# Performance work log

Hardware: AMD Instinct MI355X
Metric: run time of the kernel (lower is better)

## Reference

```python
import jax, jax.numpy as jnp
import numpy as np

N, D = 4096, 32


def setup_inputs() -> dict:
    key = jax.random.key(0)
    k1, _ = jax.random.split(key)
    particles = jax.random.normal(k1, (N, D), dtype=jnp.float32)
    length_scale = jnp.ones((1,), dtype=jnp.float32)
    return {"particles": particles, "length_scale": length_scale}


def reference(particles, length_scale):
    # SVGDModel.calculate_gradient with an RBF kernel and standard-Gaussian density.
    num_particles = particles.shape[0]
    ls2 = length_scale[0] ** 2

    # pairwise differences: diff[i, j] = x_i - x_j  -> [N, N, D]
    diff = particles[:, None, :] - particles[None, :, :]
    sq_dists = jnp.sum(diff * diff, axis=-1)               # [N, N]

    # gram_matrix = k(x_i, x_j) = exp(-||x_i - x_j||^2 / (2 l^2))
    gram_matrix = jnp.exp(-sq_dists / (2.0 * ls2))          # [N, N]

    # density.score for standard Gaussian: grad log p(x) = -x
    score_matrix = -particles                               # [N, D]

    # kernel_gradient[i, j] = grad_{x_i} k(x_i, x_j) = -(x_i - x_j)/l^2 * k
    kernel_gradient = -(diff / ls2) * gram_matrix[..., None]  # [N, N, D]

    kernel_score_term = jnp.einsum('ij,jk->ik', gram_matrix, score_matrix)  # [N, D]
    kernel_gradient_term = jnp.sum(kernel_gradient, axis=0)                 # [N, D]

    phi = (kernel_score_term + kernel_gradient_term) / num_particles
    return phi
```

## Files before the change

kernel.cpp:

```cpp
#include <hip/hip_runtime.h>

#define NPART 4096
#define DIM 32
#define LOG2E 1.44269504088896340736f

typedef _Float16 f16x8 __attribute__((ext_vector_type(8)));
typedef _Float16 f16x4 __attribute__((ext_vector_type(4)));
typedef float f32x4 __attribute__((ext_vector_type(4)));

__global__ __launch_bounds__(256) void svgd_prep_kernel(
    const float* __restrict__ X, const float* __restrict__ ls,
    float* __restrict__ m2, _Float16* __restrict__ XhP,
    _Float16* __restrict__ XlP, _Float16* __restrict__ XT,
    float* __restrict__ out) {
  const int row = blockIdx.x * 256 + threadIdx.x;

  {
    float4 z = make_float4(0.f, 0.f, 0.f, 0.f);
    float4* o4 = reinterpret_cast<float4*>(out);
#pragma unroll
    for (int q = 0; q < 8; ++q) o4[(size_t)q * 4096 + row] = z;
  }

  float v[DIM];
  const float4* xr = reinterpret_cast<const float4*>(X + (size_t)row * DIM);
#pragma unroll
  for (int q = 0; q < 8; ++q) {
    float4 a = xr[q];
    v[4 * q + 0] = a.x; v[4 * q + 1] = a.y; v[4 * q + 2] = a.z; v[4 * q + 3] = a.w;
  }
  float n = 0.f;
#pragma unroll
  for (int d = 0; d < DIM; ++d) n = fmaf(v[d], v[d], n);
  const float lsv = ls[0];
  const float inv = 1.f / (lsv * lsv);
  m2[row] = n * (0.5f * inv) * LOG2E;

  _Float16 h[DIM], l[DIM];
#pragma unroll
  for (int d = 0; d < DIM; ++d) {
    h[d] = (_Float16)v[d];
    l[d] = (_Float16)(v[d] - (float)h[d]);
  }
#pragma unroll
  for (int g = 0; g < 4; ++g) {
    f16x8 ph, pl;
#pragma unroll
    for (int e = 0; e < 8; ++e) {
      int d = (e < 4) ? (4 * g + e) : (16 + 4 * g + (e - 4));
      ph[e] = h[d];
      pl[e] = l[d];
    }
    *reinterpret_cast<f16x8*>(XhP + (size_t)row * DIM + g * 8) = ph;
    *reinterpret_cast<f16x8*>(XlP + (size_t)row * DIM + g * 8) = pl;
  }
#pragma unroll
  for (int d = 0; d < DIM; ++d) XT[(size_t)d * NPART + row] = h[d];
}

__global__ __launch_bounds__(256, 4) void svgd_fused_kernel(
    const float* __restrict__ X, const _Float16* __restrict__ XhP,
    const _Float16* __restrict__ XlP, const _Float16* __restrict__ XT,
    const float* __restrict__ ls, const float* __restrict__ m2,
    float* __restrict__ out) {
  __shared__ float sT[4][32][32];
  __shared__ float sS[4][32];

  const int tid = threadIdx.x;
  const int lane = tid & 63;
  const int g = lane >> 4;
  const int li = lane & 15;
  const int wave = tid >> 6;
  const int i0 = blockIdx.x * 32;
  const int jbase = blockIdx.y * 512 + wave * 128;

  const float lsv = ls[0];
  const float si2 = LOG2E / (lsv * lsv);

  f16x8 bh0, bl0, bh1, bl1;
  float mi0, mi1;
  {
    const int r0 = i0 + li, r1 = i0 + 16 + li;
    bh0 = *reinterpret_cast<const f16x8*>(XhP + (size_t)r0 * DIM + g * 8);
    bl0 = *reinterpret_cast<const f16x8*>(XlP + (size_t)r0 * DIM + g * 8);
    bh1 = *reinterpret_cast<const f16x8*>(XhP + (size_t)r1 * DIM + g * 8);
    bl1 = *reinterpret_cast<const f16x8*>(XlP + (size_t)r1 * DIM + g * 8);
    mi0 = m2[r0];
    mi1 = m2[r1];
  }

  f32x4 c2a0 = {0.f, 0.f, 0.f, 0.f}, c2b0 = {0.f, 0.f, 0.f, 0.f};
  f32x4 c2a1 = {0.f, 0.f, 0.f, 0.f}, c2b1 = {0.f, 0.f, 0.f, 0.f};
  float Sp0 = 0.f, Sp1 = 0.f;

  f16x8 Ah0, Al0, Ah1, Al1;
  f16x4 Ba0, Bb0, Ba1, Bb1;
  float4 Mj0, Mj1;

  auto LOADJ = [&](int j0, f16x8& Ah, f16x8& Al, f16x4& Ba, f16x4& Bb,
                   float4& Mj) {
    Ah = *reinterpret_cast<const f16x8*>(XhP + (size_t)(j0 + li) * DIM + g * 8);
    Al = *reinterpret_cast<const f16x8*>(XlP + (size_t)(j0 + li) * DIM + g * 8);
    Ba = *reinterpret_cast<const f16x4*>(XT + (size_t)li * NPART + j0 + 4 * g);
    Bb = *reinterpret_cast<const f16x4*>(XT + (size_t)(16 + li) * NPART + j0 + 4 * g);
    Mj = *reinterpret_cast<const float4*>(m2 + j0 + 4 * g);
  };

  auto COMP = [&](const f16x8& Ah, const f16x8& Al, const f16x4& Ba,
                  const f16x4& Bb, const float4& Mj) {
    f32x4 c10 = {0.f, 0.f, 0.f, 0.f}, c11 = {0.f, 0.f, 0.f, 0.f};
    c10 = __builtin_amdgcn_mfma_f32_16x16x32_f16(Ah, bh0, c10, 0, 0, 0);
    c11 = __builtin_amdgcn_mfma_f32_16x16x32_f16(Ah, bh1, c11, 0, 0, 0);
    c10 = __builtin_amdgcn_mfma_f32_16x16x32_f16(Al, bh0, c10, 0, 0, 0);
    c11 = __builtin_amdgcn_mfma_f32_16x16x32_f16(Al, bh1, c11, 0, 0, 0);
    c10 = __builtin_amdgcn_mfma_f32_16x16x32_f16(Ah, bl0, c10, 0, 0, 0);
    c11 = __builtin_amdgcn_mfma_f32_16x16x32_f16(Ah, bl1, c11, 0, 0, 0);
    const float mj[4] = {Mj.x, Mj.y, Mj.z, Mj.w};
    f16x4 a20, a21;
#pragma unroll
    for (int r = 0; r < 4; ++r) {
      float k0 = exp2f(fmaf(c10[r], si2, -(mi0 + mj[r])));
      float k1 = exp2f(fmaf(c11[r], si2, -(mi1 + mj[r])));
      Sp0 += k0;
      Sp1 += k1;
      a20[r] = (_Float16)k0;
      a21[r] = (_Float16)k1;
    }
    c2a0 = __builtin_amdgcn_mfma_f32_16x16x16f16(a20, Ba, c2a0, 0, 0, 0);
    c2b0 = __builtin_amdgcn_mfma_f32_16x16x16f16(a20, Bb, c2b0, 0, 0, 0);
    c2a1 = __builtin_amdgcn_mfma_f32_16x16x16f16(a21, Ba, c2a1, 0, 0, 0);
    c2b1 = __builtin_amdgcn_mfma_f32_16x16x16f16(a21, Bb, c2b1, 0, 0, 0);
  };

  LOADJ(jbase, Ah0, Al0, Ba0, Bb0, Mj0);
#pragma unroll
  for (int itr = 0; itr < 8; itr += 2) {
    LOADJ(jbase + (itr + 1) * 16, Ah1, Al1, Ba1, Bb1, Mj1);
    COMP(Ah0, Al0, Ba0, Bb0, Mj0);
    const int jn2 = jbase + ((itr + 2 < 8) ? (itr + 2) * 16 : 0);
    LOADJ(jn2, Ah0, Al0, Ba0, Bb0, Mj0);
    COMP(Ah1, Al1, Ba1, Bb1, Mj1);
  }

#pragma unroll
  for (int r = 0; r < 4; ++r) {
    sT[wave][4 * g + r][li] = c2a0[r];
    sT[wave][4 * g + r][16 + li] = c2b0[r];
    sT[wave][16 + 4 * g + r][li] = c2a1[r];
    sT[wave][16 + 4 * g + r][16 + li] = c2b1[r];
  }
  {
    float s0 = Sp0, s1 = Sp1;
    s0 += __shfl_xor(s0, 16, 64);
    s0 += __shfl_xor(s0, 32, 64);
    s1 += __shfl_xor(s1, 16, 64);
    s1 += __shfl_xor(s1, 32, 64);
    if (g == 0) {
      sS[wave][li] = s0;
      sS[wave][16 + li] = s1;
    }
  }
  __syncthreads();

  const float inv = si2 * (1.f / LOG2E);
  const float c1f = inv * (1.f / NPART);
  const float c2f = (1.f + inv) * (1.f / NPART);
#pragma unroll
  for (int q = 0; q < 4; ++q) {
    const int v = q * 256 + tid;
    const int row = v >> 5, d = v & 31;
    const float T = sT[0][row][d] + sT[1][row][d] + sT[2][row][d] + sT[3][row][d];
    const float S = sS[0][row] + sS[1][row] + sS[2][row] + sS[3][row];
    const size_t idx = (size_t)(i0 + row) * DIM + d;
    unsafeAtomicAdd(&out[idx], c1f * S * X[idx] - c2f * T);
  }
}

#define TJ 64
__global__ __launch_bounds__(256) void svgd_direct_kernel(const float* __restrict__ X,
                                                          const float* __restrict__ ls,
                                                          float* __restrict__ out) {
  __shared__ float4 sX[TJ * 8];
  const int tid = threadIdx.x;
  const int row = blockIdx.x * 256 + tid;
  const float lsv = ls[0];
  const float ls2 = lsv * lsv;
  const float inv2 = 0.5f / ls2;
  float4 xi[8];
  const float4* xr = reinterpret_cast<const float4*>(X + (size_t)row * DIM);
#pragma unroll
  for (int q = 0; q < 8; ++q) xi[q] = xr[q];
  float4 acc[8];
#pragma unroll
  for (int q = 0; q < 8; ++q) acc[q] = make_float4(0.f, 0.f, 0.f, 0.f);
  float S = 0.f;
  for (int jb = 0; jb < NPART; jb += TJ) {
    __syncthreads();
    const float4* src = reinterpret_cast<const float4*>(X + (size_t)jb * DIM);
    for (int t = tid; t < TJ * 8; t += 256) sX[t] = src[t];
    __syncthreads();
    for (int t = 0; t < TJ; ++t) {
      const float4* xj = &sX[t * 8];
      float4 v[8];
      float d0 = 0.f, d1 = 0.f, d2 = 0.f, d3 = 0.f;
#pragma unroll
      for (int q = 0; q < 8; ++q) {
        v[q] = xj[q];
        float ax = xi[q].x - v[q].x; d0 = fmaf(ax, ax, d0);
        float ay = xi[q].y - v[q].y; d1 = fmaf(ay, ay, d1);
        float az = xi[q].z - v[q].z; d2 = fmaf(az, az, d2);
        float aw = xi[q].w - v[q].w; d3 = fmaf(aw, aw, d3);
      }
      float k = __expf(-((d0 + d1) + (d2 + d3)) * inv2);
      S += k;
#pragma unroll
      for (int q = 0; q < 8; ++q) {
        acc[q].x = fmaf(k, v[q].x, acc[q].x);
        acc[q].y = fmaf(k, v[q].y, acc[q].y);
        acc[q].z = fmaf(k, v[q].z, acc[q].z);
        acc[q].w = fmaf(k, v[q].w, acc[q].w);
      }
    }
  }
  const float inv = 1.f / ls2;
  const float c1 = inv * S;
  const float c2 = 1.f + inv;
  float4* o = reinterpret_cast<float4*>(out + (size_t)row * DIM);
#pragma unroll
  for (int q = 0; q < 8; ++q) {
    float4 r;
    r.x = (c1 * xi[q].x - c2 * acc[q].x) * (1.f / NPART);
    r.y = (c1 * xi[q].y - c2 * acc[q].y) * (1.f / NPART);
    r.z = (c1 * xi[q].z - c2 * acc[q].z) * (1.f / NPART);
    r.w = (c1 * xi[q].w - c2 * acc[q].w) * (1.f / NPART);
    o[q] = r;
  }
}

extern "C" void kernel_launch(void* const* d_in, const int* in_sizes, int n_in,
                              void* d_out, int out_size, void* d_ws, size_t ws_size,
                              hipStream_t stream) {
  const float* X = (const float*)d_in[0];
  const float* ls = (const float*)d_in[1];
  float* out = (float*)d_out;
  float* ws = (float*)d_ws;

  const size_t fixed = 4096 + 3 * 65536;
  if (4 * fixed > ws_size) {
    svgd_direct_kernel<<<NPART / 256, 256, 0, stream>>>(X, ls, out);
    return;
  }

  float* m2 = ws;
  _Float16* XhP = reinterpret_cast<_Float16*>(ws + 4096);
  _Float16* XlP = XhP + NPART * DIM;
  _Float16* XT = XlP + NPART * DIM;

  svgd_prep_kernel<<<NPART / 256, 256, 0, stream>>>(X, ls, m2, XhP, XlP, XT, out);
  dim3 grid(NPART / 32, 8);
  svgd_fused_kernel<<<grid, 256, 0, stream>>>(X, XhP, XlP, XT, ls, m2, out);
}
```

Before: 27.29 us.

## Fuse prep into main kernel, converting j-tiles to f16 hi/lo in shared memory

Replaces the separate prep kernel with a single-pass kernel. Each block loads its j-tile of fp32 particles, computes the norms and the f16 hi/lo splits plus the transposed copy, and stages them in LDS before doing the MFMA work. The output is zeroed with hipMemsetAsync instead of by the prep kernel. This removes a kernel launch and the workspace round trip, but every block now redoes the conversion work for its j-tile (8x redundancy across blockIdx.x) and adds extra syncthreads per stage.

```diff
diff --git a/kernel.cpp b/kernel.cpp
--- a/kernel.cpp
+++ b/kernel.cpp
@@ -7,6 +7,167 @@
 typedef _Float16 f16x8 __attribute__((ext_vector_type(8)));
 typedef _Float16 f16x4 __attribute__((ext_vector_type(4)));
 typedef float f32x4 __attribute__((ext_vector_type(4)));
+
+__global__ __launch_bounds__(256, 4) void svgd_onepass_kernel(
+    const float* __restrict__ X, const float* __restrict__ ls,
+    float* __restrict__ out) {
+  __shared__ __align__(16) unsigned char smem[26624];
+  _Float16* sHi = (_Float16*)smem;
+  _Float16* sLo = (_Float16*)(smem + 8192);
+  _Float16* sXT = (_Float16*)(smem + 16384);
+  float* sM2 = (float*)(smem + 25088);
+  float* sS = (float*)(smem + 26112);
+  float* sT = (float*)smem;
+
+  const int tid = threadIdx.x;
+  const int lane = tid & 63;
+  const int g = lane >> 4;
+  const int li = lane & 15;
+  const int wave = tid >> 6;
+  const int i0 = blockIdx.x * 32;
+  const int jb0 = blockIdx.y * 512;
+
+  const float lsv = ls[0];
+  const float inv = 1.f / (lsv * lsv);
+  const float si2 = LOG2E * inv;
+  const float hm = 0.5f * si2;
+
+  const float4* X4 = (const float4*)X;
+
+  f16x8 bh0, bl0, bh1, bl1;
+  float mi0, mi1;
+  {
+    const int r0 = i0 + li, r1 = i0 + 16 + li;
+    float4 a0 = X4[(size_t)r0 * 8 + g], b0 = X4[(size_t)r0 * 8 + 4 + g];
+    float4 a1 = X4[(size_t)r1 * 8 + g], b1 = X4[(size_t)r1 * 8 + 4 + g];
+    float t0[8] = {a0.x, a0.y, a0.z, a0.w, b0.x, b0.y, b0.z, b0.w};
+    float t1[8] = {a1.x, a1.y, a1.z, a1.w, b1.x, b1.y, b1.z, b1.w};
+    float n0 = 0.f, n1 = 0.f;
+#pragma unroll
+    for (int e = 0; e < 8; ++e) {
+      n0 = fmaf(t0[e], t0[e], n0);
+      n1 = fmaf(t1[e], t1[e], n1);
+      _Float16 h0 = (_Float16)t0[e];
+      _Float16 h1 = (_Float16)t1[e];
+      bh0[e] = h0; bl0[e] = (_Float16)(t0[e] - (float)h0);
+      bh1[e] = h1; bl1[e] = (_Float16)(t1[e] - (float)h1);
+    }
+    n0 += __shfl_xor(n0, 16, 64);
+    n0 += __shfl_xor(n0, 32, 64);
+    n1 += __shfl_xor(n1, 16, 64);
+    n1 += __shfl_xor(n1, 32, 64);
+    mi0 = n0 * hm;
+    mi1 = n1 * hm;
+  }
+
+  f32x4 c2a0 = {0.f, 0.f, 0.f, 0.f}, c2b0 = {0.f, 0.f, 0.f, 0.f};
+  f32x4 c2a1 = {0.f, 0.f, 0.f, 0.f}, c2b1 = {0.f, 0.f, 0.f, 0.f};
+  float Sp0 = 0.f, Sp1 = 0.f;
+
+#pragma unroll
+  for (int s = 0; s < 4; ++s) {
+    __syncthreads();
+    {
+      const int r = tid >> 1, sub = tid & 1;
+      const int row = jb0 + s * 128 + r;
+      const float4* src = X4 + (size_t)row * 8 + sub * 4;
+      float4 va = src[0], vb = src[1], vc = src[2], vd = src[3];
+      float tv[16] = {va.x, va.y, va.z, va.w, vb.x, vb.y, vb.z, vb.w,
+                      vc.x, vc.y, vc.z, vc.w, vd.x, vd.y, vd.z, vd.w};
+      _Float16 h[16], l[16];
+      float nrm = 0.f;
+#pragma unroll
+      for (int e = 0; e < 16; ++e) {
+        nrm = fmaf(tv[e], tv[e], nrm);
+        _Float16 hh = (_Float16)tv[e];
+        h[e] = hh;
+        l[e] = (_Float16)(tv[e] - (float)hh);
+      }
+      sM2[sub * 128 + r] = nrm * hm;
+#pragma unroll
+      for (int gq = 0; gq < 4; ++gq) {
+        f16x4 ph, pl;
+#pragma unroll
+        for (int e = 0; e < 4; ++e) { ph[e] = h[4 * gq + e]; pl[e] = l[4 * gq + e]; }
+        *(f16x4*)(sHi + r * 32 + gq * 8 + sub * 4) = ph;
+        *(f16x4*)(sLo + r * 32 + gq * 8 + sub * 4) = pl;
+      }
+#pragma unroll
+      for (int e = 0; e < 16; ++e) sXT[(16 * sub + e) * 136 + r] = h[e];
+    }
+    __syncthreads();
+
+#pragma unroll
+    for (int it = 0; it < 2; ++it) {
+      const int jloc = wave * 32 + it * 16;
+      f16x8 Ah = *(const f16x8*)(sHi + (jloc + li) * 32 + g * 8);
+      f16x8 Al = *(const f16x8*)(sLo + (jloc + li) * 32 + g * 8);
+      f16x4 Ba = *(const f16x4*)(sXT + li * 136 + jloc + 4 * g);
+      f16x4 Bb = *(const f16x4*)(sXT + (16 + li) * 136 + jloc + 4 * g);
+      f32x4 Mja = *(const f32x4*)(sM2 + jloc + 4 * g);
+      f32x4 Mjb = *(const f32x4*)(sM2 + 128 + jloc + 4 * g);
+
+      f32x4 c10 = {0.f, 0.f, 0.f, 0.f}, c11 = {0.f, 0.f, 0.f, 0.f};
+      c10 = __builtin_amdgcn_mfma_f32_16x16x32_f16(Ah, bh0, c10, 0, 0, 0);
+      c11 = __builtin_amdgcn_mfma_f32_16x16x32_f16(Ah, bh1, c11, 0, 0, 0);
+      c10 = __builtin_amdgcn_mfma_f32_16x16x32_f16(Al, bh0, c10, 0, 0, 0);
+      c11 = __builtin_amdgcn_mfma_f32_16x16x32_f16(Al, bh1, c11, 0, 0, 0);
+      c10 = __builtin_amdgcn_mfma_f32_16x16x32_f16(Ah, bl0, c10, 0, 0, 0);
+      c11 = __builtin_amdgcn_mfma_f32_16x16x32_f16(Ah, bl1, c11, 0, 0, 0);
+      f16x4 a20, a21;
+#pragma unroll
+      for (int r = 0; r < 4; ++r) {
+        const float mj = Mja[r] + Mjb[r];
+        float k0 = exp2f(fmaf(c10[r], si2, -(mi0 + mj)));
+        float k1 = exp2f(fmaf(c11[r], si2, -(mi1 + mj)));
+        Sp0 += k0;
+        Sp1 += k1;
+        a20[r] = (_Float16)k0;
+        a21[r] = (_Float16)k1;
+      }
+      c2a0 = __builtin_amdgcn_mfma_f32_16x16x16f16(a20, Ba, c2a0, 0, 0, 0);
+      c2b0 = __builtin_amdgcn_mfma_f32_16x16x16f16(a20, Bb, c2b0, 0, 0, 0);
+      c2a1 = __builtin_amdgcn_mfma_f32_16x16x16f16(a21, Ba, c2a1, 0, 0, 0);
+      c2b1 = __builtin_amdgcn_mfma_f32_16x16x16f16(a21, Bb, c2b1, 0, 0, 0);
+    }
+  }
+
+  __syncthreads();
+
+#pragma unroll
+  for (int r = 0; r < 4; ++r) {
+    sT[(wave * 32 + 4 * g + r) * 32 + li] = c2a0[r];
+    sT[(wave * 32 + 4 * g + r) * 32 + 16 + li] = c2b0[r];
+    sT[(wave * 32 + 16 + 4 * g + r) * 32 + li] = c2a1[r];
+    sT[(wave * 32 + 16 + 4 * g + r) * 32 + 16 + li] = c2b1[r];
+  }
+  {
+    float s0 = Sp0, s1 = Sp1;
+    s0 += __shfl_xor(s0, 16, 64);
+    s0 += __shfl_xor(s0, 32, 64);
+    s1 += __shfl_xor(s1, 16, 64);
+    s1 += __shfl_xor(s1, 32, 64);
+    if (g == 0) {
+      sS[wave * 32 + li] = s0;
+      sS[wave * 32 + 16 + li] = s1;
+    }
+  }
+  __syncthreads();
+
+  const float c1f = inv * (1.f / NPART);
+  const float c2f = (1.f + inv) * (1.f / NPART);
+#pragma unroll
+  for (int q = 0; q < 4; ++q) {
+    const int v = q * 256 + tid;
+    const int row = v >> 5, d = v & 31;
+    const float T = sT[(0 * 32 + row) * 32 + d] + sT[(1 * 32 + row) * 32 + d] +
+                    sT[(2 * 32 + row) * 32 + d] + sT[(3 * 32 + row) * 32 + d];
+    const float S = sS[0 * 32 + row] + sS[1 * 32 + row] + sS[2 * 32 + row] +
+                    sS[3 * 32 + row];
+    const size_t idx = (size_t)(i0 + row) * DIM + d;
+    unsafeAtomicAdd(&out[idx], c1f * S * X[idx] - c2f * T);
+  }
+}
 
 __global__ __launch_bounds__(256) void svgd_prep_kernel(
     const float* __restrict__ X, const float* __restrict__ ls,
@@ -14,14 +175,12 @@
     _Float16* __restrict__ XlP, _Float16* __restrict__ XT,
     float* __restrict__ out) {
   const int row = blockIdx.x * 256 + threadIdx.x;
-
   {
     float4 z = make_float4(0.f, 0.f, 0.f, 0.f);
     float4* o4 = reinterpret_cast<float4*>(out);
 #pragma unroll
     for (int q = 0; q < 8; ++q) o4[(size_t)q * 4096 + row] = z;
   }
-
   float v[DIM];
   const float4* xr = reinterpret_cast<const float4*>(X + (size_t)row * DIM);
 #pragma unroll
@@ -35,7 +194,6 @@
   const float lsv = ls[0];
   const float inv = 1.f / (lsv * lsv);
   m2[row] = n * (0.5f * inv) * LOG2E;
-
   _Float16 h[DIM], l[DIM];
 #pragma unroll
   for (int d = 0; d < DIM; ++d) {
@@ -65,7 +223,6 @@
     float* __restrict__ out) {
   __shared__ float sT[4][32][32];
   __shared__ float sS[4][32];
-
   const int tid = threadIdx.x;
   const int lane = tid & 63;
   const int g = lane >> 4;
@@ -73,10 +230,8 @@
   const int wave = tid >> 6;
   const int i0 = blockIdx.x * 32;
   const int jbase = blockIdx.y * 512 + wave * 128;
-
   const float lsv = ls[0];
   const float si2 = LOG2E / (lsv * lsv);
-
   f16x8 bh0, bl0, bh1, bl1;
   float mi0, mi1;
   {
@@ -88,15 +243,12 @@
     mi0 = m2[r0];
     mi1 = m2[r1];
   }
-
   f32x4 c2a0 = {0.f, 0.f, 0.f, 0.f}, c2b0 = {0.f, 0.f, 0.f, 0.f};
   f32x4 c2a1 = {0.f, 0.f, 0.f, 0.f}, c2b1 = {0.f, 0.f, 0.f, 0.f};
   float Sp0 = 0.f, Sp1 = 0.f;
-
   f16x8 Ah0, Al0, Ah1, Al1;
   f16x4 Ba0, Bb0, Ba1, Bb1;
   float4 Mj0, Mj1;
-
   auto LOADJ = [&](int j0, f16x8& Ah, f16x8& Al, f16x4& Ba, f16x4& Bb,
                    float4& Mj) {
     Ah = *reinterpret_cast<const f16x8*>(XhP + (size_t)(j0 + li) * DIM + g * 8);
@@ -105,7 +257,6 @@
     Bb = *reinterpret_cast<const f16x4*>(XT + (size_t)(16 + li) * NPART + j0 + 4 * g);
     Mj = *reinterpret_cast<const float4*>(m2 + j0 + 4 * g);
   };
-
   auto COMP = [&](const f16x8& Ah, const f16x8& Al, const f16x4& Ba,
                   const f16x4& Bb, const float4& Mj) {
     f32x4 c10 = {0.f, 0.f, 0.f, 0.f}, c11 = {0.f, 0.f, 0.f, 0.f};
@@ -131,7 +282,6 @@
     c2a1 = __builtin_amdgcn_mfma_f32_16x16x16f16(a21, Ba, c2a1, 0, 0, 0);
     c2b1 = __builtin_amdgcn_mfma_f32_16x16x16f16(a21, Bb, c2b1, 0, 0, 0);
   };
-
   LOADJ(jbase, Ah0, Al0, Ba0, Bb0, Mj0);
 #pragma unroll
   for (int itr = 0; itr < 8; itr += 2) {
@@ -141,7 +291,6 @@
     LOADJ(jn2, Ah0, Al0, Ba0, Bb0, Mj0);
     COMP(Ah1, Al1, Ba1, Bb1, Mj1);
   }
-
 #pragma unroll
   for (int r = 0; r < 4; ++r) {
     sT[wave][4 * g + r][li] = c2a0[r];
@@ -161,7 +310,6 @@
     }
   }
   __syncthreads();
-
   const float inv = si2 * (1.f / LOG2E);
   const float c1f = inv * (1.f / NPART);
   const float c2f = (1.f + inv) * (1.f / NPART);
@@ -245,18 +393,25 @@
   float* out = (float*)d_out;
   float* ws = (float*)d_ws;
 
+  hipError_t e =
+      hipMemsetAsync(d_out, 0, (size_t)out_size * sizeof(float), stream);
+  if (e == hipSuccess) {
+    dim3 grid(NPART / 32, 8);
+    svgd_onepass_kernel<<<grid, 256, 0, stream>>>(X, ls, out);
+    return;
+  }
+
   const size_t fixed = 4096 + 3 * 65536;
   if (4 * fixed > ws_size) {
     svgd_direct_kernel<<<NPART / 256, 256, 0, stream>>>(X, ls, out);
     return;
   }
-
   float* m2 = ws;
   _Float16* XhP = reinterpret_cast<_Float16*>(ws + 4096);
   _Float16* XlP = XhP + NPART * DIM;
   _Float16* XT = XlP + NPART * DIM;
-
-  svgd_prep_kernel<<<NPART / 256, 256, 0, stream>>>(X, ls, m2, XhP, XlP, XT, out);
+  svgd_prep_kernel<<<NPART / 256, 256, 0, stream>>>(X, ls, m2, XhP, XlP, XT,
+                                                    out);
   dim3 grid(NPART / 32, 8);
   svgd_fused_kernel<<<grid, 256, 0, stream>>>(X, XhP, XlP, XT, ls, m2, out);
 }
```

Measured after the change: 26.63 us. 2.4% less time.

## Fuse fp16 split preprocessing into main kernel via shared-memory staging

Applied to the files above, without the earlier changes.

Drops the separate prep kernel and its workspace buffers. The main kernel now loads raw fp32 particles itself, splits each into hi/lo fp16 parts, computes squared norms, and stages j-tiles plus a transposed copy in shared memory. Output zeroing moves to a memset. The grid is also replicated REP=4 times along y with a 1/REP scale, so every j-block is computed four times and atomically added four times. That buys more blocks at the cost of redundant compute and atomics.

```diff
diff --git a/kernel.cpp b/kernel.cpp
--- a/kernel.cpp
+++ b/kernel.cpp
@@ -8,63 +8,17 @@
 typedef _Float16 f16x4 __attribute__((ext_vector_type(4)));
 typedef float f32x4 __attribute__((ext_vector_type(4)));
 
-__global__ __launch_bounds__(256) void svgd_prep_kernel(
+#define REP 4
+__global__ __launch_bounds__(256, 4) void svgd_onepass_kernel(
     const float* __restrict__ X, const float* __restrict__ ls,
-    float* __restrict__ m2, _Float16* __restrict__ XhP,
-    _Float16* __restrict__ XlP, _Float16* __restrict__ XT,
     float* __restrict__ out) {
-  const int row = blockIdx.x * 256 + threadIdx.x;
-
-  {
-    float4 z = make_float4(0.f, 0.f, 0.f, 0.f);
-    float4* o4 = reinterpret_cast<float4*>(out);
-#pragma unroll
-    for (int q = 0; q < 8; ++q) o4[(size_t)q * 4096 + row] = z;
-  }
-
-  float v[DIM];
-  const float4* xr = reinterpret_cast<const float4*>(X + (size_t)row * DIM);
-#pragma unroll
-  for (int q = 0; q < 8; ++q) {
-    float4 a = xr[q];
-    v[4 * q + 0] = a.x; v[4 * q + 1] = a.y; v[4 * q + 2] = a.z; v[4 * q + 3] = a.w;
-  }
-  float n = 0.f;
-#pragma unroll
-  for (int d = 0; d < DIM; ++d) n = fmaf(v[d], v[d], n);
-  const float lsv = ls[0];
-  const float inv = 1.f / (lsv * lsv);
-  m2[row] = n * (0.5f * inv) * LOG2E;
-
-  _Float16 h[DIM], l[DIM];
-#pragma unroll
-  for (int d = 0; d < DIM; ++d) {
-    h[d] = (_Float16)v[d];
-    l[d] = (_Float16)(v[d] - (float)h[d]);
-  }
-#pragma unroll
-  for (int g = 0; g < 4; ++g) {
-    f16x8 ph, pl;
-#pragma unroll
-    for (int e = 0; e < 8; ++e) {
-      int d = (e < 4) ? (4 * g + e) : (16 + 4 * g + (e - 4));
-      ph[e] = h[d];
-      pl[e] = l[d];
-    }
-    *reinterpret_cast<f16x8*>(XhP + (size_t)row * DIM + g * 8) = ph;
-    *reinterpret_cast<f16x8*>(XlP + (size_t)row * DIM + g * 8) = pl;
-  }
-#pragma unroll
-  for (int d = 0; d < DIM; ++d) XT[(size_t)d * NPART + row] = h[d];
-}
-
-__global__ __launch_bounds__(256, 4) void svgd_fused_kernel(
-    const float* __restrict__ X, const _Float16* __restrict__ XhP,
-    const _Float16* __restrict__ XlP, const _Float16* __restrict__ XT,
-    const float* __restrict__ ls, const float* __restrict__ m2,
-    float* __restrict__ out) {
-  __shared__ float sT[4][32][32];
-  __shared__ float sS[4][32];
+  __shared__ __align__(16) unsigned char smem[26624];
+  _Float16* sHi = (_Float16*)smem;
+  _Float16* sLo = (_Float16*)(smem + 8192);
+  _Float16* sXT = (_Float16*)(smem + 16384);
+  float* sM2 = (float*)(smem + 25088);
+  float* sS = (float*)(smem + 26112);
+  float* sT = (float*)smem;
 
   const int tid = threadIdx.x;
   const int lane = tid & 63;
@@ -72,82 +26,121 @@
   const int li = lane & 15;
   const int wave = tid >> 6;
   const int i0 = blockIdx.x * 32;
-  const int jbase = blockIdx.y * 512 + wave * 128;
+  const int jb0 = (blockIdx.y & 7) * 512;
 
   const float lsv = ls[0];
-  const float si2 = LOG2E / (lsv * lsv);
+  const float inv = 1.f / (lsv * lsv);
+  const float si2 = LOG2E * inv;
+  const float hm = 0.5f * si2;
+
+  const float4* X4 = (const float4*)X;
 
   f16x8 bh0, bl0, bh1, bl1;
   float mi0, mi1;
   {
     const int r0 = i0 + li, r1 = i0 + 16 + li;
-    bh0 = *reinterpret_cast<const f16x8*>(XhP + (size_t)r0 * DIM + g * 8);
-    bl0 = *reinterpret_cast<const f16x8*>(XlP + (size_t)r0 * DIM + g * 8);
-    bh1 = *reinterpret_cast<const f16x8*>(XhP + (size_t)r1 * DIM + g * 8);
-    bl1 = *reinterpret_cast<const f16x8*>(XlP + (size_t)r1 * DIM + g * 8);
-    mi0 = m2[r0];
-    mi1 = m2[r1];
+    float4 a0 = X4[(size_t)r0 * 8 + g], b0 = X4[(size_t)r0 * 8 + 4 + g];
+    float4 a1 = X4[(size_t)r1 * 8 + g], b1 = X4[(size_t)r1 * 8 + 4 + g];
+    float t0[8] = {a0.x, a0.y, a0.z, a0.w, b0.x, b0.y, b0.z, b0.w};
+    float t1[8] = {a1.x, a1.y, a1.z, a1.w, b1.x, b1.y, b1.z, b1.w};
+    float n0 = 0.f, n1 = 0.f;
+#pragma unroll
+    for (int e = 0; e < 8; ++e) {
+      n0 = fmaf(t0[e], t0[e], n0);
+      n1 = fmaf(t1[e], t1[e], n1);
+      _Float16 h0 = (_Float16)t0[e];
+      _Float16 h1 = (_Float16)t1[e];
+      bh0[e] = h0; bl0[e] = (_Float16)(t0[e] - (float)h0);
+      bh1[e] = h1; bl1[e] = (_Float16)(t1[e] - (float)h1);
+    }
+    n0 += __shfl_xor(n0, 16, 64);
+    n0 += __shfl_xor(n0, 32, 64);
+    n1 += __shfl_xor(n1, 16, 64);
+    n1 += __shfl_xor(n1, 32, 64);
+    mi0 = n0 * hm;
+    mi1 = n1 * hm;
   }
 
   f32x4 c2a0 = {0.f, 0.f, 0.f, 0.f}, c2b0 = {0.f, 0.f, 0.f, 0.f};
   f32x4 c2a1 = {0.f, 0.f, 0.f, 0.f}, c2b1 = {0.f, 0.f, 0.f, 0.f};
   float Sp0 = 0.f, Sp1 = 0.f;
 
-  f16x8 Ah0, Al0, Ah1, Al1;
-  f16x4 Ba0, Bb0, Ba1, Bb1;
-  float4 Mj0, Mj1;
-
-  auto LOADJ = [&](int j0, f16x8& Ah, f16x8& Al, f16x4& Ba, f16x4& Bb,
-                   float4& Mj) {
-    Ah = *reinterpret_cast<const f16x8*>(XhP + (size_t)(j0 + li) * DIM + g * 8);
-    Al = *reinterpret_cast<const f16x8*>(XlP + (size_t)(j0 + li) * DIM + g * 8);
-    Ba = *reinterpret_cast<const f16x4*>(XT + (size_t)li * NPART + j0 + 4 * g);
-    Bb = *reinterpret_cast<const f16x4*>(XT + (size_t)(16 + li) * NPART + j0 + 4 * g);
-    Mj = *reinterpret_cast<const float4*>(m2 + j0 + 4 * g);
-  };
-
-  auto COMP = [&](const f16x8& Ah, const f16x8& Al, const f16x4& Ba,
-                  const f16x4& Bb, const float4& Mj) {
-    f32x4 c10 = {0.f, 0.f, 0.f, 0.f}, c11 = {0.f, 0.f, 0.f, 0.f};
-    c10 = __builtin_amdgcn_mfma_f32_16x16x32_f16(Ah, bh0, c10, 0, 0, 0);
-    c11 = __builtin_amdgcn_mfma_f32_16x16x32_f16(Ah, bh1, c11, 0, 0, 0);
-    c10 = __builtin_amdgcn_mfma_f32_16x16x32_f16(Al, bh0, c10, 0, 0, 0);
-    c11 = __builtin_amdgcn_mfma_f32_16x16x32_f16(Al, bh1, c11, 0, 0, 0);
-    c10 = __builtin_amdgcn_mfma_f32_16x16x32_f16(Ah, bl0, c10, 0, 0, 0);
-    c11 = __builtin_amdgcn_mfma_f32_16x16x32_f16(Ah, bl1, c11, 0, 0, 0);
-    const float mj[4] = {Mj.x, Mj.y, Mj.z, Mj.w};
-    f16x4 a20, a21;
-#pragma unroll
-    for (int r = 0; r < 4; ++r) {
-      float k0 = exp2f(fmaf(c10[r], si2, -(mi0 + mj[r])));
-      float k1 = exp2f(fmaf(c11[r], si2, -(mi1 + mj[r])));
-      Sp0 += k0;
-      Sp1 += k1;
-      a20[r] = (_Float16)k0;
-      a21[r] = (_Float16)k1;
-    }
-    c2a0 = __builtin_amdgcn_mfma_f32_16x16x16f16(a20, Ba, c2a0, 0, 0, 0);
-    c2b0 = __builtin_amdgcn_mfma_f32_16x16x16f16(a20, Bb, c2b0, 0, 0, 0);
-    c2a1 = __builtin_amdgcn_mfma_f32_16x16x16f16(a21, Ba, c2a1, 0, 0, 0);
-    c2b1 = __builtin_amdgcn_mfma_f32_16x16x16f16(a21, Bb, c2b1, 0, 0, 0);
-  };
-
-  LOADJ(jbase, Ah0, Al0, Ba0, Bb0, Mj0);
-#pragma unroll
-  for (int itr = 0; itr < 8; itr += 2) {
-    LOADJ(jbase + (itr + 1) * 16, Ah1, Al1, Ba1, Bb1, Mj1);
-    COMP(Ah0, Al0, Ba0, Bb0, Mj0);
-    const int jn2 = jbase + ((itr + 2 < 8) ? (itr + 2) * 16 : 0);
-    LOADJ(jn2, Ah0, Al0, Ba0, Bb0, Mj0);
-    COMP(Ah1, Al1, Ba1, Bb1, Mj1);
-  }
+#pragma unroll
+  for (int s = 0; s < 4; ++s) {
+    __syncthreads();
+    {
+      const int r = tid >> 1, sub = tid & 1;
+      const int row = jb0 + s * 128 + r;
+      const float4* src = X4 + (size_t)row * 8 + sub * 4;
+      float4 va = src[0], vb = src[1], vc = src[2], vd = src[3];
+      float tv[16] = {va.x, va.y, va.z, va.w, vb.x, vb.y, vb.z, vb.w,
+                      vc.x, vc.y, vc.z, vc.w, vd.x, vd.y, vd.z, vd.w};
+      _Float16 h[16], l[16];
+      float nrm = 0.f;
+#pragma unroll
+      for (int e = 0; e < 16; ++e) {
+        nrm = fmaf(tv[e], tv[e], nrm);
+        _Float16 hh = (_Float16)tv[e];
+        h[e] = hh;
+        l[e] = (_Float16)(tv[e] - (float)hh);
+      }
+      sM2[sub * 128 + r] = nrm * hm;
+#pragma unroll
+      for (int gq = 0; gq < 4; ++gq) {
+        f16x4 ph, pl;
+#pragma unroll
+        for (int e = 0; e < 4; ++e) { ph[e] = h[4 * gq + e]; pl[e] = l[4 * gq + e]; }
+        *(f16x4*)(sHi + r * 32 + gq * 8 + sub * 4) = ph;
+        *(f16x4*)(sLo + r * 32 + gq * 8 + sub * 4) = pl;
+      }
+#pragma unroll
+      for (int e = 0; e < 16; ++e) sXT[(16 * sub + e) * 136 + r] = h[e];
+    }
+    __syncthreads();
+
+#pragma unroll
+    for (int it = 0; it < 2; ++it) {
+      const int jloc = wave * 32 + it * 16;
+      f16x8 Ah = *(const f16x8*)(sHi + (jloc + li) * 32 + g * 8);
+      f16x8 Al = *(const f16x8*)(sLo + (jloc + li) * 32 + g * 8);
+      f16x4 Ba = *(const f16x4*)(sXT + li * 136 + jloc + 4 * g);
+      f16x4 Bb = *(const f16x4*)(sXT + (16 + li) * 136 + jloc + 4 * g);
+      f32x4 Mja = *(const f32x4*)(sM2 + jloc + 4 * g);
+      f32x4 Mjb = *(const f32x4*)(sM2 + 128 + jloc + 4 * g);
+
+      f32x4 c10 = {0.f, 0.f, 0.f, 0.f}, c11 = {0.f, 0.f, 0.f, 0.f};
+      c10 = __builtin_amdgcn_mfma_f32_16x16x32_f16(Ah, bh0, c10, 0, 0, 0);
+      c11 = __builtin_amdgcn_mfma_f32_16x16x32_f16(Ah, bh1, c11, 0, 0, 0);
+      c10 = __builtin_amdgcn_mfma_f32_16x16x32_f16(Al, bh0, c10, 0, 0, 0);
+      c11 = __builtin_amdgcn_mfma_f32_16x16x32_f16(Al, bh1, c11, 0, 0, 0);
+      c10 = __builtin_amdgcn_mfma_f32_16x16x32_f16(Ah, bl0, c10, 0, 0, 0);
+      c11 = __builtin_amdgcn_mfma_f32_16x16x32_f16(Ah, bl1, c11, 0, 0, 0);
+      f16x4 a20, a21;
+#pragma unroll
+      for (int r = 0; r < 4; ++r) {
+        const float mj = Mja[r] + Mjb[r];
+        float k0 = exp2f(fmaf(c10[r], si2, -(mi0 + mj)));
+        float k1 = exp2f(fmaf(c11[r], si2, -(mi1 + mj)));
+        Sp0 += k0;
+        Sp1 += k1;
+        a20[r] = (_Float16)k0;
+        a21[r] = (_Float16)k1;
+      }
+      c2a0 = __builtin_amdgcn_mfma_f32_16x16x16f16(a20, Ba, c2a0, 0, 0, 0);
+      c2b0 = __builtin_amdgcn_mfma_f32_16x16x16f16(a20, Bb, c2b0, 0, 0, 0);
+      c2a1 = __builtin_amdgcn_mfma_f32_16x16x16f16(a21, Ba, c2a1, 0, 0, 0);
+      c2b1 = __builtin_amdgcn_mfma_f32_16x16x16f16(a21, Bb, c2b1, 0, 0, 0);
+    }
+  }
+
+  __syncthreads();
 
 #pragma unroll
   for (int r = 0; r < 4; ++r) {
-    sT[wave][4 * g + r][li] = c2a0[r];
-    sT[wave][4 * g + r][16 + li] = c2b0[r];
-    sT[wave][16 + 4 * g + r][li] = c2a1[r];
-    sT[wave][16 + 4 * g + r][16 + li] = c2b1[r];
+    sT[(wave * 32 + 4 * g + r) * 32 + li] = c2a0[r];
+    sT[(wave * 32 + 4 * g + r) * 32 + 16 + li] = c2b0[r];
+    sT[(wave * 32 + 16 + 4 * g + r) * 32 + li] = c2a1[r];
+    sT[(wave * 32 + 16 + 4 * g + r) * 32 + 16 + li] = c2b1[r];
   }
   {
     float s0 = Sp0, s1 = Sp1;
@@ -156,21 +149,22 @@
     s1 += __shfl_xor(s1, 16, 64);
     s1 += __shfl_xor(s1, 32, 64);
     if (g == 0) {
-      sS[wave][li] = s0;
-      sS[wave][16 + li] = s1;
+      sS[wave * 32 + li] = s0;
+      sS[wave * 32 + 16 + li] = s1;
     }
   }
   __syncthreads();
 
-  const float inv = si2 * (1.f / LOG2E);
-  const float c1f = inv * (1.f / NPART);
-  const float c2f = (1.f + inv) * (1.f / NPART);
+  const float c1f = inv * (1.f / NPART) * (1.f / REP);
+  const float c2f = (1.f + inv) * (1.f / NPART) * (1.f / REP);
 #pragma unroll
   for (int q = 0; q < 4; ++q) {
     const int v = q * 256 + tid;
     const int row = v >> 5, d = v & 31;
-    const float T = sT[0][row][d] + sT[1][row][d] + sT[2][row][d] + sT[3][row][d];
-    const float S = sS[0][row] + sS[1][row] + sS[2][row] + sS[3][row];
+    const float T = sT[(0 * 32 + row) * 32 + d] + sT[(1 * 32 + row) * 32 + d] +
+                    sT[(2 * 32 + row) * 32 + d] + sT[(3 * 32 + row) * 32 + d];
+    const float S = sS[0 * 32 + row] + sS[1 * 32 + row] + sS[2 * 32 + row] +
+                    sS[3 * 32 + row];
     const size_t idx = (size_t)(i0 + row) * DIM + d;
     unsafeAtomicAdd(&out[idx], c1f * S * X[idx] - c2f * T);
   }
@@ -243,20 +237,15 @@
   const float* X = (const float*)d_in[0];
   const float* ls = (const float*)d_in[1];
   float* out = (float*)d_out;
-  float* ws = (float*)d_ws;
-
-  const size_t fixed = 4096 + 3 * 65536;
-  if (4 * fixed > ws_size) {
-    svgd_direct_kernel<<<NPART / 256, 256, 0, stream>>>(X, ls, out);
+  (void)d_ws;
+  (void)ws_size;
+
+  hipError_t e =
+      hipMemsetAsync(d_out, 0, (size_t)out_size * sizeof(float), stream);
+  if (e == hipSuccess) {
+    dim3 grid(NPART / 32, 8 * REP);
+    svgd_onepass_kernel<<<grid, 256, 0, stream>>>(X, ls, out);
     return;
   }
-
-  float* m2 = ws;
-  _Float16* XhP = reinterpret_cast<_Float16*>(ws + 4096);
-  _Float16* XlP = XhP + NPART * DIM;
-  _Float16* XT = XlP + NPART * DIM;
-
-  svgd_prep_kernel<<<NPART / 256, 256, 0, stream>>>(X, ls, m2, XhP, XlP, XT, out);
-  dim3 grid(NPART / 32, 8);
-  svgd_fused_kernel<<<grid, 256, 0, stream>>>(X, XhP, XlP, XT, ls, m2, out);
+  svgd_direct_kernel<<<NPART / 256, 256, 0, stream>>>(X, ls, out);
 }
```

New measurement: 65.11 us. 139% more time.
